# Kernel optimization log

Hardware: AMD Instinct MI355X
Metric: run time of the kernel (lower is better)

The kernel has to match this reference:

```python
import jax, jax.numpy as jnp
import numpy as np

EMB = 2048
NH = 16
HD = EMB // NH
EPS = 1e-5


def setup_inputs() -> dict:
    key = jax.random.key(0)
    ks = jax.random.split(key, 16)
    s = 1.0 / np.sqrt(EMB)
    def lin(k, din, dout):
        return jax.random.normal(k, (din, dout), jnp.float32) * (1.0 / np.sqrt(din))
    return {
        "embeddings": jax.random.normal(ks[0], (2, 2048, EMB), jnp.float32),
        "Wq": lin(ks[1], EMB, EMB), "bq": jnp.zeros((EMB,), jnp.float32),
        "Wk": lin(ks[2], EMB, EMB), "bk": jnp.zeros((EMB,), jnp.float32),
        "Wv": lin(ks[3], EMB, EMB), "bv": jnp.zeros((EMB,), jnp.float32),
        "Wfc": lin(ks[4], EMB, EMB), "bfc": jnp.zeros((EMB,), jnp.float32),
        "g1": jnp.ones((EMB,), jnp.float32), "be1": jnp.zeros((EMB,), jnp.float32),
        "W1": lin(ks[5], EMB, 4 * EMB), "b1": jnp.zeros((4 * EMB,), jnp.float32),
        "W2": lin(ks[6], 4 * EMB, EMB), "b2": jnp.zeros((EMB,), jnp.float32),
        "g2": jnp.ones((EMB,), jnp.float32), "be2": jnp.zeros((EMB,), jnp.float32),
    }


def _layernorm(x, g, b):
    mu = jnp.mean(x, axis=-1, keepdims=True)
    var = jnp.mean(jnp.square(x - mu), axis=-1, keepdims=True)
    return (x - mu) * jax.lax.rsqrt(var + EPS) * g + b


def reference(embeddings, Wq, bq, Wk, bk, Wv, bv, Wfc, bfc, g1, be1, W1, b1, W2, b2, g2, be2):
    B, S, E = embeddings.shape
    old = embeddings
    # QKV projections, split heads: [B, H, S, D]
    def heads(x):
        return x.reshape(B, S, NH, HD).transpose(0, 2, 1, 3)
    q = heads(embeddings @ Wq + bq)
    k = heads(embeddings @ Wk + bk)
    v = heads(embeddings @ Wv + bv)
    # naive causal attention: full [B,H,S,S] scores (faithful to source)
    scores = jnp.einsum("bhsd,bhtd->bhst", q, k) / np.sqrt(HD)
    causal = jnp.triu(jnp.full((S, S), -jnp.inf, jnp.float32), k=1)
    scores = scores + causal[None, None]
    attn = jax.nn.softmax(scores, axis=-1)
    ctx = jnp.einsum("bhst,bhtd->bhsd", attn, v)
    ctx = ctx.transpose(0, 2, 1, 3).reshape(B, S, E)
    # dropout is identity in eval mode
    x = ctx @ Wfc + bfc + old
    old = _layernorm(x, g1, be1)
    h = jax.nn.gelu(old @ W1 + b1, approximate=False)
    x = h @ W2 + b2 + old
    return _layernorm(x, g2, be2)
```

## Files before the change

kernel.cpp:

```cpp
#include <hip/hip_runtime.h>
#include <hip/hip_bf16.h>
#include <math.h>

#define EMB  2048
#define NH   16
#define HD   128
#define SEQ  2048
#define BATCH 2
#define MTOK (BATCH*SEQ)

using bf16x8 = __attribute__((ext_vector_type(8))) __bf16;
using f32x4  = __attribute__((ext_vector_type(4))) float;

__device__ __forceinline__ unsigned short f2bf(float x) {
    unsigned int u = __float_as_uint(x);
    u += 0x7fffu + ((u >> 16) & 1u);
    return (unsigned short)(u >> 16);
}
__device__ __forceinline__ float bf2f(unsigned int u16) {
    return __uint_as_float(u16 << 16);
}

__device__ __forceinline__ float gelu_exact(float x) {
    return 0.5f * x * (1.0f + erff(x * 0.70710678118654752f));
}

__global__ __launch_bounds__(256) void k_conv(const float* __restrict__ in,
                                              unsigned short* __restrict__ out, int n4) {
    int i = blockIdx.x * 256 + threadIdx.x;
    if (i >= n4) return;
    float4 v = ((const float4*)in)[i];
    ushort4 o;
    o.x = f2bf(v.x); o.y = f2bf(v.y); o.z = f2bf(v.z); o.w = f2bf(v.w);
    ((ushort4*)out)[i] = o;
}

__global__ __launch_bounds__(256) void k_transconv(const float* __restrict__ W,
                                                   unsigned short* __restrict__ Wt,
                                                   int K, int N) {
    __shared__ float t[32][33];
    int tx = threadIdx.x & 31, ty = threadIdx.x >> 5;
    int c0 = blockIdx.x * 32, r0 = blockIdx.y * 32;
    #pragma unroll
    for (int i = 0; i < 4; ++i)
        t[ty + i*8][tx] = W[(size_t)(r0 + ty + i*8) * N + c0 + tx];
    __syncthreads();
    #pragma unroll
    for (int i = 0; i < 4; ++i)
        Wt[(size_t)(c0 + ty + i*8) * K + r0 + tx] = f2bf(t[tx][ty + i*8]);
}

template<int EPI, int NSPLIT>
__global__ __launch_bounds__(512, 4) void k_gemm5(const unsigned short* __restrict__ A,
                                                  const unsigned short* __restrict__ Bt,
                                                  const float* __restrict__ bias,
                                                  void* __restrict__ C0,
                                                  void* __restrict__ C1,
                                                  int M, int N, int Kred, int ldk) {
    __shared__ unsigned short As[3][256 * 32];
    __shared__ unsigned short Bs[3][128 * 32];
    const int tid = threadIdx.x, lane = tid & 63, wid = tid >> 6;
    const int la15 = lane & 15, g = lane >> 4;
    const int wm = wid >> 1, wn = wid & 1;
    const int nmt = M >> 8, nnt = N >> 7;
    const int ncol = (nnt * NSPLIT) >> 3;
    const int xcd = blockIdx.x & 7;
    const int i4 = blockIdx.x >> 3;
    const int bmg = i4 / (ncol << 2);
    const int j4 = i4 - bmg * (ncol << 2);
    const int bm = (bmg << 2) + (j4 & 3);
    const int colg = xcd * ncol + (j4 >> 2);
    const int bn = colg % nnt, kk2 = colg / nnt;
    const unsigned short* Ab = A  + (size_t)bm * 256 * ldk + (size_t)kk2 * Kred;
    const unsigned short* Bb = Bt + (size_t)bn * 128 * ldk + (size_t)kk2 * Kred;

    auto STAGE = [&](int ti, int bbuf) {
        const int kt = ti * 32;
        #pragma unroll
        for (int it = 0; it < 2; ++it) {
            const int slot = it * 512 + tid;
            const int r = slot >> 2, pos = slot & 3;
            const unsigned short* ga = Ab + (size_t)r * ldk + kt
                                     + ((pos ^ ((r >> 1) & 3)) * 8);
            __builtin_amdgcn_global_load_lds(
                (const __attribute__((address_space(1))) void*)ga,
                (__attribute__((address_space(3))) void*)&As[bbuf][(it*512 + wid*64) * 8], 16, 0, 0);
        }
        {
            const int r = tid >> 2, pos = tid & 3;
            const unsigned short* gb = Bb + (size_t)r * ldk + kt
                                     + ((pos ^ ((r >> 1) & 3)) * 8);
            __builtin_amdgcn_global_load_lds(
                (const __attribute__((address_space(1))) void*)gb,
                (__attribute__((address_space(3))) void*)&Bs[bbuf][(size_t)wid * 64 * 8], 16, 0, 0);
        }
    };

    f32x4 acc[4][4] = {};
    const int NT = Kred >> 5;
    STAGE(0, 0);
    STAGE(1, 1);
    STAGE(2, 2);

    int cur = 0;
    for (int t = 0; t < NT; ++t) {
        if (t + 2 < NT)      asm volatile("s_waitcnt vmcnt(6)" ::: "memory");
        else if (t + 1 < NT) asm volatile("s_waitcnt vmcnt(3)" ::: "memory");
        else                 asm volatile("s_waitcnt vmcnt(0)" ::: "memory");
        __builtin_amdgcn_s_barrier();
        __builtin_amdgcn_sched_barrier(0);

        bf16x8 af[4], bfr[4];
        #pragma unroll
        for (int mi = 0; mi < 4; ++mi) {
            const int r = wm*64 + mi*16 + la15;
            af[mi] = *(const bf16x8*)&As[cur][r*32 + ((g ^ ((r >> 1) & 3)) * 8)];
        }
        #pragma unroll
        for (int ni = 0; ni < 4; ++ni) {
            const int r = wn*64 + ni*16 + la15;
            bfr[ni] = *(const bf16x8*)&Bs[cur][r*32 + ((g ^ ((r >> 1) & 3)) * 8)];
        }
        __builtin_amdgcn_s_setprio(1);
        #pragma unroll
        for (int mi = 0; mi < 4; ++mi)
            #pragma unroll
            for (int ni = 0; ni < 4; ++ni)
                acc[mi][ni] = __builtin_amdgcn_mfma_f32_16x16x32_bf16(af[mi], bfr[ni], acc[mi][ni], 0, 0, 0);
        __builtin_amdgcn_s_setprio(0);
        __builtin_amdgcn_sched_barrier(0);
        __builtin_amdgcn_s_barrier();
        __builtin_amdgcn_sched_barrier(0);
        if (t + 3 < NT) STAGE(t + 3, cur);
        cur = (cur == 2) ? 0 : cur + 1;
    }

    const int row0b = bm*256 + wm*64, col0 = bn*128 + wn*64;
    #pragma unroll
    for (int mi = 0; mi < 4; ++mi) {
        #pragma unroll
        for (int ni = 0; ni < 4; ++ni) {
            const int c = col0 + ni*16 + la15;
            const int r0 = row0b + mi*16 + g * 4;
            if (EPI == 5) {
                unsigned short* out = (unsigned short*)C0 + (size_t)kk2 * M * N;
                #pragma unroll
                for (int j = 0; j < 4; ++j)
                    out[(size_t)(r0+j) * N + c] = f2bf(acc[mi][ni][j]);
            } else if (EPI == 2) {
                const float bv = bias[c];
                #pragma unroll
                for (int j = 0; j < 4; ++j)
                    ((unsigned short*)C0)[(size_t)(r0+j) * N + c] = f2bf(gelu_exact(acc[mi][ni][j] + bv));
            } else if (EPI == 7) {
                const float bv = bias[c];
                const int seg = c >> 11;
                if (seg == 0) {
                    #pragma unroll
                    for (int j = 0; j < 4; ++j)
                        ((unsigned short*)C0)[(size_t)(r0+j) * EMB + c] = f2bf(acc[mi][ni][j] + bv);
                } else {
                    #pragma unroll
                    for (int j = 0; j < 4; ++j)
                        ((unsigned short*)C1)[(size_t)(r0+j) * EMB + (c - 2048)] = f2bf(acc[mi][ni][j] + bv);
                }
            } else {
                const int hh = c >> 7, dd = c & 127;
                const int bb2 = r0 >> 11, s0 = r0 & 2047;
                unsigned short* out = (unsigned short*)C0 + (size_t)kk2 * ((size_t)MTOK * EMB);
                ushort4 uo;
                uo.x = f2bf(acc[mi][ni][0]); uo.y = f2bf(acc[mi][ni][1]);
                uo.z = f2bf(acc[mi][ni][2]); uo.w = f2bf(acc[mi][ni][3]);
                *(ushort4*)(out + ((size_t)((bb2*NH + hh)*HD + dd) * SEQ + s0)) = uo;
            }
        }
    }
}

__global__ __launch_bounds__(256) void k_vcomb(const unsigned short* __restrict__ a,
                                               const unsigned short* __restrict__ b,
                                               const float* __restrict__ bv,
                                               unsigned short* __restrict__ vt) {
    const int i8 = blockIdx.x * 256 + threadIdx.x;
    const float bias = bv[(i8 >> 8) & 2047];
    uint4 ua = ((const uint4*)a)[i8];
    uint4 ub = ((const uint4*)b)[i8];
    const unsigned int* pa = (const unsigned int*)&ua;
    const unsigned int* pb = (const unsigned int*)&ub;
    uint4 uo;
    unsigned int* po = (unsigned int*)&uo;
    #pragma unroll
    for (int i = 0; i < 4; ++i) {
        const unsigned short lo = f2bf(bf2f(pa[i] & 0xffffu) + bf2f(pb[i] & 0xffffu) + bias);
        const unsigned short hi = f2bf(bf2f(pa[i] >> 16)     + bf2f(pb[i] >> 16)     + bias);
        po[i] = (unsigned int)lo | ((unsigned int)hi << 16);
    }
    ((uint4*)vt)[i8] = uo;
}

__global__ __launch_bounds__(256, 4) void k_attn_part(const unsigned short* __restrict__ Qb,
                                                      const unsigned short* __restrict__ Kb,
                                                      const unsigned short* __restrict__ VTb,
                                                      unsigned short* __restrict__ Opart,
                                                      float* __restrict__ Ml) {
    const int tid = threadIdx.x;
    const int lane = tid & 63, w = tid >> 6;
    const int g = lane >> 4, c = lane & 15;
    const int bid = blockIdx.x;
    const int swz = (bid & 7) * 512 + (bid >> 3);
    const int bh = swz >> 7;
    const int b = bh >> 4, h = bh & 15;
    const int rr = swz & 127;
    const int qt = rr >> 2, ks = rr & 3;
    const int nt = qt + 1;
    const int t0 = (nt * ks) >> 2, t1 = (nt * (ks + 1)) >> 2;
    const int qb = qt * 64 + w * 16;

    __shared__ unsigned short Ks[64 * 128];
    __shared__ unsigned short Vs[128 * 64];
    __shared__ unsigned short p_lds[4][16 * 64];

    bf16x8 qf[4];
    {
        const unsigned short* qrow = Qb + (size_t)(b*SEQ + qb + c) * EMB + h*HD;
        #pragma unroll
        for (int dch = 0; dch < 4; ++dch)
            qf[dch] = *(const bf16x8*)(qrow + dch*32 + g*8);
    }

    f32x4 o[8];
    #pragma unroll
    for (int ni = 0; ni < 8; ++ni) o[ni] = (f32x4){0.f, 0.f, 0.f, 0.f};
    float m_c = -1e30f, l_c = 0.f;

    const int q = qb + c;
    const int qmaxw = qb + 15;
    const unsigned short* Kbase = Kb  + (size_t)(b*SEQ) * EMB + h*HD;
    const unsigned short* Vbase = VTb + (size_t)((b*NH + h) * HD) * SEQ;
    const float scale = 0.08838834764831845f;
    char* pw = (char*)&p_lds[w][0];

    for (int ti = t0; ti < t1; ++ti) {
        const int tc = ti * 64;
        #pragma unroll
        for (int it = 0; it < 4; ++it) {
            const int cl = it * 256 + tid;
            const unsigned short* gk = Kbase + (size_t)(tc + (cl >> 4)) * EMB
                                     + (((cl & 15) ^ ((cl >> 4) & 7)) * 8);
            __builtin_amdgcn_global_load_lds(
                (const __attribute__((address_space(1))) void*)gk,
                (__attribute__((address_space(3))) void*)&Ks[(it*256 + w*64) * 8], 16, 0, 0);
            const unsigned short* gv = Vbase + (size_t)(cl >> 3) * SEQ + tc
                                     + (((cl & 7) ^ ((cl >> 3) & 7)) * 8);
            __builtin_amdgcn_global_load_lds(
                (const __attribute__((address_space(1))) void*)gv,
                (__attribute__((address_space(3))) void*)&Vs[(it*256 + w*64) * 8], 16, 0, 0);
        }
        __syncthreads();

        f32x4 sc[4];
        #pragma unroll
        for (int kt = 0; kt < 4; ++kt) {
            sc[kt] = (f32x4){0.f, 0.f, 0.f, 0.f};
            if (tc + kt*16 <= qmaxw) {
                #pragma unroll
                for (int dch = 0; dch < 4; ++dch) {
                    bf16x8 kf = *(const bf16x8*)&Ks[(kt*16 + c)*128 + (((dch*4 + g) ^ (c & 7)) * 8)];
                    sc[kt] = __builtin_amdgcn_mfma_f32_16x16x32_bf16(kf, qf[dch], sc[kt], 0, 0, 0);
                }
            }
        }
        float mx = -1e30f;
        #pragma unroll
        for (int kt = 0; kt < 4; ++kt)
            #pragma unroll
            for (int j = 0; j < 4; ++j) {
                const int key = tc + kt*16 + g*4 + j;
                const float s = (key <= q) ? sc[kt][j] * scale : -1e30f;
                mx = fmaxf(mx, s);
            }
        mx = fmaxf(mx, __shfl_xor(mx, 16));
        mx = fmaxf(mx, __shfl_xor(mx, 32));
        if (!__all(mx <= m_c + 8.f)) {
            const float mn = fmaxf(m_c, mx);
            const float corr = __expf(m_c - mn);
            l_c *= corr;
            m_c = mn;
            #pragma unroll
            for (int j = 0; j < 4; ++j) {
                const float cj = __shfl(corr, g*4 + j);
                #pragma unroll
                for (int ni = 0; ni < 8; ++ni) o[ni][j] *= cj;
            }
        }
        float ps = 0.f;
        #pragma unroll
        for (int kt = 0; kt < 4; ++kt) {
            float p[4];
            #pragma unroll
            for (int j = 0; j < 4; ++j) {
                const int key = tc + kt*16 + g*4 + j;
                const float s = (key <= q) ? sc[kt][j] * scale : -1e30f;
                p[j] = __expf(s - m_c);
                ps += p[j];
            }
            uint2 pk;
            pk.x = (unsigned int)f2bf(p[0]) | ((unsigned int)f2bf(p[1]) << 16);
            pk.y = (unsigned int)f2bf(p[2]) | ((unsigned int)f2bf(p[3]) << 16);
            const int byte = (c*128 + kt*32 + g*8) ^ ((c & 7) << 4);
            *(uint2*)(pw + byte) = pk;
        }
        ps += __shfl_xor(ps, 16);
        ps += __shfl_xor(ps, 32);
        l_c += ps;
        asm volatile("s_waitcnt lgkmcnt(0)" ::: "memory");
        __builtin_amdgcn_sched_barrier(0);
        #pragma unroll
        for (int kc = 0; kc < 2; ++kc) {
            if (tc + kc*32 <= qmaxw) {
                const int byte = (c*128 + kc*64 + g*16) ^ ((c & 7) << 4);
                bf16x8 pa = *(const bf16x8*)(pw + byte);
                #pragma unroll
                for (int ni = 0; ni < 8; ++ni) {
                    bf16x8 vf = *(const bf16x8*)&Vs[(ni*16 + c)*64 + (((kc*4 + g) ^ (c & 7)) * 8)];
                    o[ni] = __builtin_amdgcn_mfma_f32_16x16x32_bf16(pa, vf, o[ni], 0, 0, 0);
                }
            }
        }
        __syncthreads();
    }

    const int slot = ((b*NH + h) * 32 + qt) * 4 + ks;
    unsigned short* op = Opart + (size_t)slot * (64 * 128);
    #pragma unroll
    for (int ni = 0; ni < 8; ++ni)
        #pragma unroll
        for (int j = 0; j < 4; ++j)
            op[(size_t)(w*16 + g*4 + j) * 128 + ni*16 + c] = f2bf(o[ni][j]);
    if (lane < 16) {
        Ml[(size_t)slot * 128 +      w*16 + lane] = m_c;
        Ml[(size_t)slot * 128 + 64 + w*16 + lane] = l_c;
    }
}

__global__ __launch_bounds__(256) void k_attn_reduce(const unsigned short* __restrict__ Opart,
                                                     const float* __restrict__ Ml,
                                                     unsigned short* __restrict__ Ob) {
    const int qt = blockIdx.x, h = blockIdx.y, b = blockIdx.z;
    const int slot0 = ((b*NH + h) * 32 + qt) * 4;
    const int row = threadIdx.x >> 2;
    const int c0 = (threadIdx.x & 3) * 32;
    float M = -1e30f;
    #pragma unroll
    for (int s = 0; s < 4; ++s)
        M = fmaxf(M, Ml[(size_t)(slot0 + s) * 128 + row]);
    float L = 0.f;
    float wgt[4];
    #pragma unroll
    for (int s = 0; s < 4; ++s) {
        wgt[s] = __expf(Ml[(size_t)(slot0 + s) * 128 + row] - M);
        L += Ml[(size_t)(slot0 + s) * 128 + 64 + row] * wgt[s];
    }
    float acc[32];
    #pragma unroll
    for (int k = 0; k < 32; ++k) acc[k] = 0.f;
    #pragma unroll
    for (int s = 0; s < 4; ++s) {
        const unsigned short* op = Opart + ((size_t)(slot0 + s) * 64 + row) * 128 + c0;
        #pragma unroll
        for (int q4 = 0; q4 < 4; ++q4) {
            uint4 u = ((const uint4*)op)[q4];
            const unsigned int* pu = (const unsigned int*)&u;
            #pragma unroll
            for (int k = 0; k < 4; ++k) {
                acc[q4*8 + 2*k]     += bf2f(pu[k] & 0xffffu) * wgt[s];
                acc[q4*8 + 2*k + 1] += bf2f(pu[k] >> 16)     * wgt[s];
            }
        }
    }
    const float inv = 1.0f / L;
    unsigned short* orow = Ob + (size_t)(b*SEQ + qt*64 + row) * EMB + h*HD + c0;
    #pragma unroll
    for (int q4 = 0; q4 < 8; ++q4) {
        ushort4 u;
        u.x = f2bf(acc[q4*4+0] * inv); u.y = f2bf(acc[q4*4+1] * inv);
        u.z = f2bf(acc[q4*4+2] * inv); u.w = f2bf(acc[q4*4+3] * inv);
        ((ushort4*)orow)[q4] = u;
    }
}

__global__ __launch_bounds__(256) void k_lnb(const unsigned short* __restrict__ X0,
                                             const unsigned short* __restrict__ X1,
                                             const float* __restrict__ bias,
                                             const float* __restrict__ resF,
                                             const unsigned short* __restrict__ resB,
                                             const float* __restrict__ g,
                                             const float* __restrict__ be,
                                             float* __restrict__ Of32,
                                             unsigned short* __restrict__ Obf16) {
    const int row = blockIdx.x, t = threadIdx.x;
    float v[8];
    {
        uint4 a = ((const uint4*)(X0 + (size_t)row * EMB))[t];
        uint4 b = ((const uint4*)(X1 + (size_t)row * EMB))[t];
        const unsigned int* pa = (const unsigned int*)&a;
        const unsigned int* pb = (const unsigned int*)&b;
        #pragma unroll
        for (int i = 0; i < 4; ++i) {
            v[2*i]   = bf2f(pa[i] & 0xffffu) + bf2f(pb[i] & 0xffffu);
            v[2*i+1] = bf2f(pa[i] >> 16)     + bf2f(pb[i] >> 16);
        }
    }
    {
        float4 b0 = ((const float4*)bias)[t*2], b1 = ((const float4*)bias)[t*2+1];
        v[0] += b0.x; v[1] += b0.y; v[2] += b0.z; v[3] += b0.w;
        v[4] += b1.x; v[5] += b1.y; v[6] += b1.z; v[7] += b1.w;
    }
    if (resF) {
        float4 r0 = ((const float4*)(resF + (size_t)row * EMB))[t*2];
        float4 r1 = ((const float4*)(resF + (size_t)row * EMB))[t*2+1];
        v[0] += r0.x; v[1] += r0.y; v[2] += r0.z; v[3] += r0.w;
        v[4] += r1.x; v[5] += r1.y; v[6] += r1.z; v[7] += r1.w;
    }
    if (resB) {
        uint4 r = ((const uint4*)(resB + (size_t)row * EMB))[t];
        const unsigned int* pr = (const unsigned int*)&r;
        #pragma unroll
        for (int i = 0; i < 4; ++i) {
            v[2*i]   += bf2f(pr[i] & 0xffffu);
            v[2*i+1] += bf2f(pr[i] >> 16);
        }
    }
    float s = 0.f, ss = 0.f;
    #pragma unroll
    for (int i = 0; i < 8; ++i) { s += v[i]; ss += v[i]*v[i]; }
    #pragma unroll
    for (int o = 32; o; o >>= 1) { s += __shfl_xor(s, o); ss += __shfl_xor(ss, o); }
    __shared__ float red[2][4];
    const int lane = t & 63, wid = t >> 6;
    if (lane == 0) { red[0][wid] = s; red[1][wid] = ss; }
    __syncthreads();
    s  = red[0][0] + red[0][1] + red[0][2] + red[0][3];
    ss = red[1][0] + red[1][1] + red[1][2] + red[1][3];
    const float mu = s * (1.0f / EMB);
    const float var = ss * (1.0f / EMB) - mu * mu;
    const float rs = rsqrtf(var + 1e-5f);
    float y[8];
    {
        float4 g0 = ((const float4*)g)[t*2],  g1v = ((const float4*)g)[t*2+1];
        float4 e0 = ((const float4*)be)[t*2], e1 = ((const float4*)be)[t*2+1];
        const float* pg0 = (const float*)&g0; const float* pg1 = (const float*)&g1v;
        const float* pe0 = (const float*)&e0; const float* pe1 = (const float*)&e1;
        #pragma unroll
        for (int i = 0; i < 4; ++i) {
            y[i]   = (v[i]   - mu) * rs * pg0[i] + pe0[i];
            y[i+4] = (v[i+4] - mu) * rs * pg1[i] + pe1[i];
        }
    }
    if (Of32) {
        float4 o0, o1;
        o0.x = y[0]; o0.y = y[1]; o0.z = y[2]; o0.w = y[3];
        o1.x = y[4]; o1.y = y[5]; o1.z = y[6]; o1.w = y[7];
        ((float4*)(Of32 + (size_t)row * EMB))[t*2]   = o0;
        ((float4*)(Of32 + (size_t)row * EMB))[t*2+1] = o1;
    }
    if (Obf16) {
        uint4 u;
        unsigned int* pu = (unsigned int*)&u;
        #pragma unroll
        for (int i = 0; i < 4; ++i)
            pu[i] = (unsigned int)f2bf(y[2*i]) | ((unsigned int)f2bf(y[2*i+1]) << 16);
        ((uint4*)(Obf16 + (size_t)row * EMB))[t] = u;
    }
}

extern "C" void kernel_launch(void* const* d_in, const int* in_sizes, int n_in,
                              void* d_out, int out_size, void* d_ws, size_t ws_size,
                              hipStream_t stream) {
    const float* emb = (const float*)d_in[0];
    const float* Wq  = (const float*)d_in[1];  const float* bq  = (const float*)d_in[2];
    const float* Wk  = (const float*)d_in[3];  const float* bk  = (const float*)d_in[4];
    const float* Wv  = (const float*)d_in[5];  const float* bv  = (const float*)d_in[6];
    const float* Wfc = (const float*)d_in[7];  const float* bfc = (const float*)d_in[8];
    const float* g1  = (const float*)d_in[9];  const float* be1 = (const float*)d_in[10];
    const float* W1  = (const float*)d_in[11]; const float* b1  = (const float*)d_in[12];
    const float* W2  = (const float*)d_in[13]; const float* b2  = (const float*)d_in[14];
    const float* g2  = (const float*)d_in[15]; const float* be2 = (const float*)d_in[16];

    char* ws = (char*)d_ws;
    unsigned short* aB   = (unsigned short*)(ws + (size_t)  0 * (1u<<20));
    unsigned short* ln1B = (unsigned short*)(ws + (size_t) 16 * (1u<<20));
    unsigned short* WtB  = (unsigned short*)(ws + (size_t) 32 * (1u<<20));
    float*          Ml   = (float*)         (ws + (size_t) 32 * (1u<<20));
    unsigned short* hB   = (unsigned short*)(ws + (size_t) 64 * (1u<<20));
    unsigned short* Qb   = (unsigned short*)(ws + (size_t) 64 * (1u<<20));
    unsigned short* Kb   = (unsigned short*)(ws + (size_t) 80 * (1u<<20));
    unsigned short* VTb  = (unsigned short*)(ws + (size_t) 96 * (1u<<20));
    unsigned short* Opart= (unsigned short*)(ws + (size_t)112 * (1u<<20));
    unsigned short* pA   = (unsigned short*)(ws + (size_t)176 * (1u<<20));
    unsigned short* pVT  = (unsigned short*)(ws + (size_t)176 * (1u<<20));
    float*          bias4= (float*)         (ws + (size_t)236 * (1u<<20));

    const dim3 blk(256);
    const dim3 blk2(512);
    const int n4 = MTOK * EMB / 4;
    const size_t PVT = (size_t)MTOK * EMB;

    k_conv<<<dim3(n4 / 256), blk, 0, stream>>>(emb, aB, n4);
    hipMemcpyAsync(bias4,       bq, EMB*sizeof(float), hipMemcpyDeviceToDevice, stream);
    hipMemcpyAsync(bias4 + EMB, bk, EMB*sizeof(float), hipMemcpyDeviceToDevice, stream);

    k_transconv<<<dim3(EMB/32, EMB/32), blk, 0, stream>>>(Wq, WtB,             EMB, EMB);
    k_transconv<<<dim3(EMB/32, EMB/32), blk, 0, stream>>>(Wk, WtB + EMB*EMB,   EMB, EMB);
    k_transconv<<<dim3(EMB/32, EMB/32), blk, 0, stream>>>(Wv, WtB + 2*EMB*EMB, EMB, EMB);
    k_gemm5<7,1><<<dim3((MTOK/256)*(2*EMB/128)), blk2, 0, stream>>>(
        aB, WtB, bias4, Qb, Kb, MTOK, 2*EMB, EMB, EMB);
    k_gemm5<8,2><<<dim3((MTOK/256)*(EMB/128)*2), blk2, 0, stream>>>(
        aB, WtB + 2*EMB*EMB, nullptr, pVT, nullptr, MTOK, EMB, EMB/2, EMB);
    k_vcomb<<<dim3((int)(PVT/8/256)), blk, 0, stream>>>(pVT, pVT + PVT, bv, VTb);

    k_attn_part<<<dim3(4096), blk, 0, stream>>>(Qb, Kb, VTb, Opart, Ml);
    k_attn_reduce<<<dim3(SEQ/64, NH, BATCH), blk, 0, stream>>>(Opart, Ml, aB);

    k_transconv<<<dim3(EMB/32, EMB/32), blk, 0, stream>>>(Wfc, WtB, EMB, EMB);
    k_gemm5<5,2><<<dim3((MTOK/256)*(EMB/128)*2), blk2, 0, stream>>>(
        aB, WtB, nullptr, pA, nullptr, MTOK, EMB, EMB/2, EMB);
    k_lnb<<<dim3(MTOK), blk, 0, stream>>>(pA, pA + (size_t)MTOK*EMB, bfc, emb, nullptr,
                                          g1, be1, nullptr, ln1B);

    k_transconv<<<dim3(4*EMB/32, EMB/32), blk, 0, stream>>>(W1, WtB, EMB, 4*EMB);
    k_gemm5<2,1><<<dim3((MTOK/256)*(4*EMB/128)), blk2, 0, stream>>>(
        ln1B, WtB, b1, hB, nullptr, MTOK, 4*EMB, EMB, EMB);

    k_transconv<<<dim3(EMB/32, (4*EMB)/32), blk, 0, stream>>>(W2, WtB, 4*EMB, EMB);
    k_gemm5<5,2><<<dim3((MTOK/256)*(EMB/128)*2), blk2, 0, stream>>>(
        hB, WtB, nullptr, pA, nullptr, MTOK, EMB, 2*EMB, 4*EMB);
    k_lnb<<<dim3(MTOK), blk, 0, stream>>>(pA, pA + (size_t)MTOK*EMB, b2, nullptr, ln1B,
                                          g2, be2, (float*)d_out, nullptr);
}
```

Baseline: 656.4 us.

## Shrink GEMM tiles to 128x128 with 256 threads and double buffering

Changes the bf16 MFMA GEMM from a 256x128 tile with 512 threads and a three-stage LDS pipeline to a 128x128 tile with 256 threads and a two-stage pipeline. The block swizzle is adjusted to group 8 row-tiles per XCD column, and all GEMM launches double their grid size. This lowers LDS use per block and creates more blocks, which could raise occupancy and balance load. The cost is lower data reuse per tile and a shallower prefetch depth, so more memory latency may be exposed.

```diff
diff --git a/kernel.cpp b/kernel.cpp
--- a/kernel.cpp
+++ b/kernel.cpp
@@ -51,48 +51,50 @@
 }
 
 template<int EPI, int NSPLIT>
-__global__ __launch_bounds__(512, 4) void k_gemm5(const unsigned short* __restrict__ A,
+__global__ __launch_bounds__(256, 4) void k_gemm6(const unsigned short* __restrict__ A,
                                                   const unsigned short* __restrict__ Bt,
                                                   const float* __restrict__ bias,
                                                   void* __restrict__ C0,
                                                   void* __restrict__ C1,
                                                   int M, int N, int Kred, int ldk) {
-    __shared__ unsigned short As[3][256 * 32];
-    __shared__ unsigned short Bs[3][128 * 32];
+    __shared__ unsigned short As[2][128 * 32];
+    __shared__ unsigned short Bs[2][128 * 32];
     const int tid = threadIdx.x, lane = tid & 63, wid = tid >> 6;
     const int la15 = lane & 15, g = lane >> 4;
     const int wm = wid >> 1, wn = wid & 1;
-    const int nmt = M >> 8, nnt = N >> 7;
+    const int nmt = M >> 7, nnt = N >> 7;
     const int ncol = (nnt * NSPLIT) >> 3;
     const int xcd = blockIdx.x & 7;
     const int i4 = blockIdx.x >> 3;
-    const int bmg = i4 / (ncol << 2);
-    const int j4 = i4 - bmg * (ncol << 2);
-    const int bm = (bmg << 2) + (j4 & 3);
-    const int colg = xcd * ncol + (j4 >> 2);
+    const int bmg = i4 / (ncol << 3);
+    const int j8 = i4 - bmg * (ncol << 3);
+    const int bm = (bmg << 3) + (j8 & 7);
+    const int colg = xcd * ncol + (j8 >> 3);
     const int bn = colg % nnt, kk2 = colg / nnt;
-    const unsigned short* Ab = A  + (size_t)bm * 256 * ldk + (size_t)kk2 * Kred;
+    const unsigned short* Ab = A  + (size_t)bm * 128 * ldk + (size_t)kk2 * Kred;
     const unsigned short* Bb = Bt + (size_t)bn * 128 * ldk + (size_t)kk2 * Kred;
 
     auto STAGE = [&](int ti, int bbuf) {
         const int kt = ti * 32;
         #pragma unroll
         for (int it = 0; it < 2; ++it) {
-            const int slot = it * 512 + tid;
+            const int slot = it * 256 + tid;
             const int r = slot >> 2, pos = slot & 3;
             const unsigned short* ga = Ab + (size_t)r * ldk + kt
                                      + ((pos ^ ((r >> 1) & 3)) * 8);
             __builtin_amdgcn_global_load_lds(
                 (const __attribute__((address_space(1))) void*)ga,
-                (__attribute__((address_space(3))) void*)&As[bbuf][(it*512 + wid*64) * 8], 16, 0, 0);
-        }
-        {
-            const int r = tid >> 2, pos = tid & 3;
+                (__attribute__((address_space(3))) void*)&As[bbuf][(it*256 + wid*64) * 8], 16, 0, 0);
+        }
+        #pragma unroll
+        for (int it = 0; it < 2; ++it) {
+            const int slot = it * 256 + tid;
+            const int r = slot >> 2, pos = slot & 3;
             const unsigned short* gb = Bb + (size_t)r * ldk + kt
                                      + ((pos ^ ((r >> 1) & 3)) * 8);
             __builtin_amdgcn_global_load_lds(
                 (const __attribute__((address_space(1))) void*)gb,
-                (__attribute__((address_space(3))) void*)&Bs[bbuf][(size_t)wid * 64 * 8], 16, 0, 0);
+                (__attribute__((address_space(3))) void*)&Bs[bbuf][(it*256 + wid*64) * 8], 16, 0, 0);
         }
     };
 
@@ -100,13 +102,11 @@
     const int NT = Kred >> 5;
     STAGE(0, 0);
     STAGE(1, 1);
-    STAGE(2, 2);
-
-    int cur = 0;
+
     for (int t = 0; t < NT; ++t) {
-        if (t + 2 < NT)      asm volatile("s_waitcnt vmcnt(6)" ::: "memory");
-        else if (t + 1 < NT) asm volatile("s_waitcnt vmcnt(3)" ::: "memory");
-        else                 asm volatile("s_waitcnt vmcnt(0)" ::: "memory");
+        const int bb = t & 1;
+        if (t + 1 < NT) asm volatile("s_waitcnt vmcnt(4)" ::: "memory");
+        else            asm volatile("s_waitcnt vmcnt(0)" ::: "memory");
         __builtin_amdgcn_s_barrier();
         __builtin_amdgcn_sched_barrier(0);
 
@@ -114,12 +114,12 @@
         #pragma unroll
         for (int mi = 0; mi < 4; ++mi) {
             const int r = wm*64 + mi*16 + la15;
-            af[mi] = *(const bf16x8*)&As[cur][r*32 + ((g ^ ((r >> 1) & 3)) * 8)];
+            af[mi] = *(const bf16x8*)&As[bb][r*32 + ((g ^ ((r >> 1) & 3)) * 8)];
         }
         #pragma unroll
         for (int ni = 0; ni < 4; ++ni) {
             const int r = wn*64 + ni*16 + la15;
-            bfr[ni] = *(const bf16x8*)&Bs[cur][r*32 + ((g ^ ((r >> 1) & 3)) * 8)];
+            bfr[ni] = *(const bf16x8*)&Bs[bb][r*32 + ((g ^ ((r >> 1) & 3)) * 8)];
         }
         __builtin_amdgcn_s_setprio(1);
         #pragma unroll
@@ -131,11 +131,10 @@
         __builtin_amdgcn_sched_barrier(0);
         __builtin_amdgcn_s_barrier();
         __builtin_amdgcn_sched_barrier(0);
-        if (t + 3 < NT) STAGE(t + 3, cur);
-        cur = (cur == 2) ? 0 : cur + 1;
-    }
-
-    const int row0b = bm*256 + wm*64, col0 = bn*128 + wn*64;
+        if (t + 2 < NT) STAGE(t + 2, bb);
+    }
+
+    const int row0b = bm*128 + wm*64, col0 = bn*128 + wn*64;
     #pragma unroll
     for (int mi = 0; mi < 4; ++mi) {
         #pragma unroll
@@ -502,7 +501,6 @@
     float*          bias4= (float*)         (ws + (size_t)236 * (1u<<20));
 
     const dim3 blk(256);
-    const dim3 blk2(512);
     const int n4 = MTOK * EMB / 4;
     const size_t PVT = (size_t)MTOK * EMB;
 
@@ -513,9 +511,9 @@
     k_transconv<<<dim3(EMB/32, EMB/32), blk, 0, stream>>>(Wq, WtB,             EMB, EMB);
     k_transconv<<<dim3(EMB/32, EMB/32), blk, 0, stream>>>(Wk, WtB + EMB*EMB,   EMB, EMB);
     k_transconv<<<dim3(EMB/32, EMB/32), blk, 0, stream>>>(Wv, WtB + 2*EMB*EMB, EMB, EMB);
-    k_gemm5<7,1><<<dim3((MTOK/256)*(2*EMB/128)), blk2, 0, stream>>>(
+    k_gemm6<7,1><<<dim3((MTOK/128)*(2*EMB/128)), blk, 0, stream>>>(
         aB, WtB, bias4, Qb, Kb, MTOK, 2*EMB, EMB, EMB);
-    k_gemm5<8,2><<<dim3((MTOK/256)*(EMB/128)*2), blk2, 0, stream>>>(
+    k_gemm6<8,2><<<dim3((MTOK/128)*(EMB/128)*2), blk, 0, stream>>>(
         aB, WtB + 2*EMB*EMB, nullptr, pVT, nullptr, MTOK, EMB, EMB/2, EMB);
     k_vcomb<<<dim3((int)(PVT/8/256)), blk, 0, stream>>>(pVT, pVT + PVT, bv, VTb);
 
@@ -523,17 +521,17 @@
     k_attn_reduce<<<dim3(SEQ/64, NH, BATCH), blk, 0, stream>>>(Opart, Ml, aB);
 
     k_transconv<<<dim3(EMB/32, EMB/32), blk, 0, stream>>>(Wfc, WtB, EMB, EMB);
-    k_gemm5<5,2><<<dim3((MTOK/256)*(EMB/128)*2), blk2, 0, stream>>>(
+    k_gemm6<5,2><<<dim3((MTOK/128)*(EMB/128)*2), blk, 0, stream>>>(
         aB, WtB, nullptr, pA, nullptr, MTOK, EMB, EMB/2, EMB);
     k_lnb<<<dim3(MTOK), blk, 0, stream>>>(pA, pA + (size_t)MTOK*EMB, bfc, emb, nullptr,
                                           g1, be1, nullptr, ln1B);
 
     k_transconv<<<dim3(4*EMB/32, EMB/32), blk, 0, stream>>>(W1, WtB, EMB, 4*EMB);
-    k_gemm5<2,1><<<dim3((MTOK/256)*(4*EMB/128)), blk2, 0, stream>>>(
+    k_gemm6<2,1><<<dim3((MTOK/128)*(4*EMB/128)), blk, 0, stream>>>(
         ln1B, WtB, b1, hB, nullptr, MTOK, 4*EMB, EMB, EMB);
 
     k_transconv<<<dim3(EMB/32, (4*EMB)/32), blk, 0, stream>>>(W2, WtB, 4*EMB, EMB);
-    k_gemm5<5,2><<<dim3((MTOK/256)*(EMB/128)*2), blk2, 0, stream>>>(
+    k_gemm6<5,2><<<dim3((MTOK/128)*(EMB/128)*2), blk, 0, stream>>>(
         hB, WtB, nullptr, pA, nullptr, MTOK, EMB, 2*EMB, 4*EMB);
     k_lnb<<<dim3(MTOK), blk, 0, stream>>>(pA, pA + (size_t)MTOK*EMB, b2, nullptr, ln1B,
                                           g2, be2, (float*)d_out, nullptr);
```

Result: slower. 719.3 us (+9.6%).
